# Kernel optimization log

Hardware: AMD Instinct MI355X
Metric: run time of the kernel (lower is better)

The kernel has to match this reference:

```python
import jax, jax.numpy as jnp
import numpy as np

WZ, WH, WW = 2, 6, 12          # window_size
NW = 64                        # type_of_windows = (8//2)*(96//6)
HEADS = 12
DIM = 384
B_ = 15                        # batch(1) * num_lon_windows(180//12)
N = WZ * WH * WW               # 144 tokens per window


def _construct_position_index():
    zi = np.arange(WZ); zj = -np.arange(WZ) * WZ
    hi = np.arange(WH); hj = -np.arange(WH) * WH
    w = np.arange(WW)
    c1 = np.stack(np.meshgrid(zi, hi, w, indexing='ij')).reshape(3, -1)
    c2 = np.stack(np.meshgrid(zj, hj, w, indexing='ij')).reshape(3, -1)
    coords = (c1[:, :, None] - c2[:, None, :]).transpose(1, 2, 0)  # (N, N, 3)
    coords[..., 2] += WW - 1
    coords[..., 1] *= 2 * WW - 1
    coords[..., 0] *= (2 * WW - 1) * WH * WH
    return coords.sum(-1).reshape(-1).astype(np.int32)  # (N*N,)


def setup_inputs() -> dict:
    key = jax.random.key(0)
    ks = jax.random.split(key, 6)
    bias_rows = (2 * WW - 1) * WH * WH * WZ * WZ  # 3312
    return {
        'x': jax.random.normal(ks[0], (B_, NW, N, DIM), dtype=jnp.float32),
        'mask': jnp.zeros((B_, N, N), dtype=jnp.float32),
        'w_qkv': jax.random.normal(ks[1], (DIM, 3 * DIM), dtype=jnp.float32) * 0.02,
        'b_qkv': jnp.zeros((3 * DIM,), dtype=jnp.float32),
        'w_proj': jax.random.normal(ks[2], (DIM, DIM), dtype=jnp.float32) * 0.02,
        'b_proj': jnp.zeros((DIM,), dtype=jnp.float32),
        'bias_table': jax.random.normal(ks[3], (bias_rows, NW, HEADS), dtype=jnp.float32) * 0.02,
        'position_index': jnp.asarray(_construct_position_index()),
    }


def reference(x, mask, w_qkv, b_qkv, w_proj, b_proj, bias_table, position_index):
    b_, nw, n, c = x.shape
    hd = c // HEADS
    scale = hd ** -0.5
    qkv = (x @ w_qkv + b_qkv).reshape(b_, nw, n, 3, HEADS, hd)
    q, k, v = jnp.moveaxis(qkv, 3, 0)            # each (B_, nW, N, H, hd)
    attn = jnp.einsum('bwnhd,bwmhd->bwhnm', q * scale, k)  # (B_, nW, H, N, N)
    # earth-specific relative bias gather: (N*N, nW, H) -> (nW, H, N, N)
    bias = bias_table[position_index].reshape(n, n, nw, HEADS).transpose(2, 3, 0, 1)
    attn = attn + bias[None]                     # broadcast over B_
    attn = attn + mask[:, None, None, :, :]      # additive mask per lon window
    attn = jax.nn.softmax(attn, axis=-1)         # dropout_rate=0 -> identity
    out = jnp.einsum('bwhnm,bwmhd->bwnhd', attn, v).reshape(b_, nw, n, c)
    return out @ w_proj + b_proj
```

## Files before the change

### kernel.cpp

```cpp
#include <hip/hip_runtime.h>
#include <cstdint>


typedef _Float16 f16;
typedef _Float16 f16x8 __attribute__((ext_vector_type(8)));
typedef _Float16 f16x4v __attribute__((ext_vector_type(4)));
typedef float f32x4 __attribute__((ext_vector_type(4)));

#define NW_ 64
#define HEADS_ 12
#define DIM_ 384
#define BATCH_ 15
#define NTOK_ 144
#define HD_ 32
#define MTOK_ (BATCH_*NW_*NTOK_)
#define NWH_ (BATCH_*NW_*HEADS_)

__device__ __forceinline__ void load16_lds(const void* g, void* l) {
    __builtin_amdgcn_global_load_lds(
        (const __attribute__((address_space(1))) uint32_t*)g,
        (__attribute__((address_space(3))) uint32_t*)l,
        16, 0, 0);
}

__device__ __forceinline__ f32x4 fzero4() {
    f32x4 z; z[0]=0.f; z[1]=0.f; z[2]=0.f; z[3]=0.f; return z;
}

__global__ void cvt_f32_to_f16(const float* __restrict__ src, f16* __restrict__ dst, int n4) {
    int i = blockIdx.x * blockDim.x + threadIdx.x;
    int stride = gridDim.x * blockDim.x;
    for (; i < n4; i += stride) {
        float4 v = ((const float4*)src)[i];
        f16x4v o;
        o[0] = (f16)v.x; o[1] = (f16)v.y; o[2] = (f16)v.z; o[3] = (f16)v.w;
        *(f16x4v*)(dst + 4*(size_t)i) = o;
    }
}

__global__ void transpose_cvt(const float* __restrict__ src, f16* __restrict__ dst, int K, int N) {
    int i = blockIdx.x * blockDim.x + threadIdx.x;
    if (i >= K*N) return;
    int n = i / K;
    int k = i - n*K;
    dst[i] = (f16)src[k*N + n];
}

__global__ __launch_bounds__(256) void qkv_gemm(
    const f16* __restrict__ A, const f16* __restrict__ Bt,
    const float* __restrict__ bias,
    f16* __restrict__ qws, f16* __restrict__ kws, f16* __restrict__ vws)
{
    constexpr int BK = 32;
    __shared__ __align__(16) f16 Asm[128*BK];
    __shared__ __align__(16) f16 Bsm[128*BK];
    const int tid  = threadIdx.x;
    const int lane = tid & 63;
    const int wave = tid >> 6;
    const int l15  = lane & 15;
    const int quad = lane >> 4;
    const int wr = wave >> 1, wc = wave & 1;
    const int row0 = blockIdx.x * 128;
    const int col0 = blockIdx.y * 128;

    f32x4 acc[4][4];
    #pragma unroll
    for (int i = 0; i < 4; ++i)
        #pragma unroll
        for (int j = 0; j < 4; ++j) acc[i][j] = fzero4();

    for (int kt = 0; kt < DIM_/BK; ++kt) {
        const int k0 = kt * BK;
        __syncthreads();
        #pragma unroll
        for (int cc = 0; cc < 2; ++cc) {
            int chunk  = wave*2 + cc;
            int flat16 = chunk*64 + lane;
            int r   = flat16 >> 2;
            int c16 = flat16 & 3;
            load16_lds(&A [(size_t)(row0 + r)*DIM_ + k0 + c16*8], (char*)Asm + (size_t)chunk*1024);
            load16_lds(&Bt[(size_t)(col0 + r)*DIM_ + k0 + c16*8], (char*)Bsm + (size_t)chunk*1024);
        }
        __syncthreads();

        f16x8 af[4], bf[4];
        #pragma unroll
        for (int i = 0; i < 4; ++i)
            af[i] = *(const f16x8*)&Asm[(wr*64 + i*16 + l15)*BK + quad*8];
        #pragma unroll
        for (int j = 0; j < 4; ++j)
            bf[j] = *(const f16x8*)&Bsm[(wc*64 + j*16 + l15)*BK + quad*8];
        #pragma unroll
        for (int i = 0; i < 4; ++i)
            #pragma unroll
            for (int j = 0; j < 4; ++j)
                acc[i][j] = __builtin_amdgcn_mfma_f32_16x16x32_f16(af[i], bf[j], acc[i][j], 0, 0, 0);
    }

    const int which = col0 / DIM_;
    #pragma unroll
    for (int j = 0; j < 4; ++j) {
        int col = col0 + wc*64 + j*16 + l15;
        float bq = bias[col];
        int rem = col - which*DIM_;
        int h = rem >> 5, d = rem & 31;
        #pragma unroll
        for (int i = 0; i < 4; ++i) {
            int rowb = row0 + wr*64 + i*16 + quad*4;
            #pragma unroll
            for (int r = 0; r < 4; ++r) {
                int row = rowb + r;
                int bw  = row / NTOK_;
                int n   = row - bw*NTOK_;
                int head = bw*HEADS_ + h;
                f16 hv = (f16)(acc[i][j][r] + bq);
                if (which == 0)      qws[(size_t)head*NTOK_*HD_ + n*HD_ + d] = hv;
                else if (which == 1) kws[(size_t)head*NTOK_*HD_ + n*HD_ + d] = hv;
                else                 vws[(size_t)head*HD_*NTOK_ + d*NTOK_ + n] = hv;
            }
        }
    }
}

__global__ __launch_bounds__(576) void attention(
    const f16* __restrict__ qws, const f16* __restrict__ kws, const f16* __restrict__ vws,
    const float* __restrict__ bias_table, const int* __restrict__ pos_idx,
    const float* __restrict__ mask, f16* __restrict__ ows)
{
    constexpr int KPAD = 40;
    constexpr int VPAD = 168;
    __shared__ __align__(16) char smem[10752 + 48384];
    f16* Vt  = (f16*)smem;
    f16* Ksm = (f16*)(smem + 10752);
    f16* Pst = (f16*)(smem + 10752);

    const int tid  = threadIdx.x;
    const int lane = tid & 63;
    const int wv   = tid >> 6;
    const int l15  = lane & 15;
    const int quad = lane >> 4;

    const int wh = blockIdx.x;
    const int w  = wh / HEADS_;
    const int h  = wh - w*HEADS_;

    float brg[9][4];
    #pragma unroll
    for (int j = 0; j < 9; ++j) {
        int m = j*16 + l15;
        #pragma unroll
        for (int r = 0; r < 4; ++r) {
            int n = wv*16 + quad*4 + r;
            int idx = pos_idx[n*NTOK_ + m];
            brg[j][r] = bias_table[(size_t)idx*(NW_*HEADS_) + w*HEADS_ + h];
        }
    }

    if (tid < 64) {
        int d = tid >> 1, m0 = 144 + (tid & 1)*8;
        uint4 z = {0u,0u,0u,0u};
        *(uint4*)&Vt[d*VPAD + m0] = z;
    }

    const float scale = 0.17677669529663687f;

    for (int b = 0; b < BATCH_; ++b) {
        const int bwh = (b*NW_ + w)*HEADS_ + h;
        const f16* qh = qws + (size_t)bwh*NTOK_*HD_;
        const f16* kh = kws + (size_t)bwh*NTOK_*HD_;
        const f16* vh = vws + (size_t)bwh*HD_*NTOK_;

        __syncthreads();
        {
            int flat = tid*8;
            int n = flat >> 5, d = flat & 31;
            *(uint4*)&Ksm[n*KPAD + d] = *(const uint4*)&kh[flat];
            int dv = flat / NTOK_;
            int mv = flat - dv*NTOK_;
            *(uint4*)&Vt[dv*VPAD + mv] = *(const uint4*)&vh[flat];
        }
        int nq = wv*16 + l15;
        f16x8 qf = *(const f16x8*)&qh[nq*HD_ + quad*8];
        __syncthreads();

        f32x4 sfr[9];
        #pragma unroll
        for (int j = 0; j < 9; ++j) {
            f16x8 kf = *(const f16x8*)&Ksm[(j*16 + l15)*KPAD + quad*8];
            sfr[j] = __builtin_amdgcn_mfma_f32_16x16x32_f16(qf, kf, fzero4(), 0, 0, 0);
        }
        __syncthreads();

        float p[9][4], rmax[4], rsum[4];
        #pragma unroll
        for (int r = 0; r < 4; ++r) rmax[r] = -1e30f;
        const float* mrow = mask + (size_t)b*NTOK_*NTOK_;
        #pragma unroll
        for (int j = 0; j < 9; ++j) {
            int m = j*16 + l15;
            #pragma unroll
            for (int r = 0; r < 4; ++r) {
                int n = wv*16 + quad*4 + r;
                float s = sfr[j][r]*scale + brg[j][r] + mrow[n*NTOK_ + m];
                p[j][r] = s;
                rmax[r] = fmaxf(rmax[r], s);
            }
        }
        #pragma unroll
        for (int r = 0; r < 4; ++r) {
            float v = rmax[r];
            #pragma unroll
            for (int off = 1; off < 16; off <<= 1)
                v = fmaxf(v, __shfl_xor(v, off, 64));
            rmax[r] = v;
        }
        #pragma unroll
        for (int r = 0; r < 4; ++r) rsum[r] = 0.f;
        #pragma unroll
        for (int j = 0; j < 9; ++j)
            #pragma unroll
            for (int r = 0; r < 4; ++r) {
                float e = __expf(p[j][r] - rmax[r]);
                p[j][r] = e;
                rsum[r] += e;
            }
        #pragma unroll
        for (int r = 0; r < 4; ++r) {
            float v = rsum[r];
            #pragma unroll
            for (int off = 1; off < 16; off <<= 1)
                v += __shfl_xor(v, off, 64);
            rsum[r] = 1.0f / v;
        }

        f16* Pw = Pst + wv*16*VPAD;
        #pragma unroll
        for (int j = 0; j < 9; ++j) {
            int m = j*16 + l15;
            #pragma unroll
            for (int r = 0; r < 4; ++r)
                Pw[(quad*4 + r)*VPAD + m] = (f16)(p[j][r]*rsum[r]);
        }
        if (lane < 32) {
            int row = lane >> 1, m0 = 144 + (lane & 1)*8;
            uint4 z = {0u,0u,0u,0u};
            *(uint4*)&Pw[row*VPAD + m0] = z;
        }

        f32x4 o0 = fzero4(), o1 = fzero4();
        #pragma unroll
        for (int s = 0; s < 5; ++s) {
            f16x8 pa = *(const f16x8*)&Pw[l15*VPAD + s*32 + quad*8];
            f16x8 v0 = *(const f16x8*)&Vt[l15*VPAD + s*32 + quad*8];
            f16x8 v1 = *(const f16x8*)&Vt[(16 + l15)*VPAD + s*32 + quad*8];
            o0 = __builtin_amdgcn_mfma_f32_16x16x32_f16(pa, v0, o0, 0, 0, 0);
            o1 = __builtin_amdgcn_mfma_f32_16x16x32_f16(pa, v1, o1, 0, 0, 0);
        }

        const int bw = b*NW_ + w;
        #pragma unroll
        for (int r = 0; r < 4; ++r) {
            int n = wv*16 + quad*4 + r;
            size_t base = ((size_t)bw*NTOK_ + n)*DIM_ + h*HD_;
            ows[base + l15]      = (f16)o0[r];
            ows[base + 16 + l15] = (f16)o1[r];
        }
    }
}

__global__ __launch_bounds__(256) void proj_gemm(
    const f16* __restrict__ A, const f16* __restrict__ Bt,
    const float* __restrict__ bias, float* __restrict__ out)
{
    constexpr int BK = 32;
    __shared__ __align__(16) f16 Asm[128*BK];
    __shared__ __align__(16) f16 Bsm[128*BK];
    const int tid  = threadIdx.x;
    const int lane = tid & 63;
    const int wave = tid >> 6;
    const int l15  = lane & 15;
    const int quad = lane >> 4;
    const int wr = wave >> 1, wc = wave & 1;
    const int row0 = blockIdx.x * 128;
    const int col0 = blockIdx.y * 128;

    f32x4 acc[4][4];
    #pragma unroll
    for (int i = 0; i < 4; ++i)
        #pragma unroll
        for (int j = 0; j < 4; ++j) acc[i][j] = fzero4();

    for (int kt = 0; kt < DIM_/BK; ++kt) {
        const int k0 = kt * BK;
        __syncthreads();
        #pragma unroll
        for (int cc = 0; cc < 2; ++cc) {
            int chunk  = wave*2 + cc;
            int flat16 = chunk*64 + lane;
            int r   = flat16 >> 2;
            int c16 = flat16 & 3;
            load16_lds(&A [(size_t)(row0 + r)*DIM_ + k0 + c16*8], (char*)Asm + (size_t)chunk*1024);
            load16_lds(&Bt[(size_t)(col0 + r)*DIM_ + k0 + c16*8], (char*)Bsm + (size_t)chunk*1024);
        }
        __syncthreads();

        f16x8 af[4], bf[4];
        #pragma unroll
        for (int i = 0; i < 4; ++i)
            af[i] = *(const f16x8*)&Asm[(wr*64 + i*16 + l15)*BK + quad*8];
        #pragma unroll
        for (int j = 0; j < 4; ++j)
            bf[j] = *(const f16x8*)&Bsm[(wc*64 + j*16 + l15)*BK + quad*8];
        #pragma unroll
        for (int i = 0; i < 4; ++i)
            #pragma unroll
            for (int j = 0; j < 4; ++j)
                acc[i][j] = __builtin_amdgcn_mfma_f32_16x16x32_f16(af[i], bf[j], acc[i][j], 0, 0, 0);
    }

    #pragma unroll
    for (int j = 0; j < 4; ++j) {
        int col = col0 + wc*64 + j*16 + l15;
        float bp = bias[col];
        #pragma unroll
        for (int i = 0; i < 4; ++i) {
            int rowb = row0 + wr*64 + i*16 + quad*4;
            #pragma unroll
            for (int r = 0; r < 4; ++r)
                out[(size_t)(rowb + r)*DIM_ + col] = acc[i][j][r] + bp;
        }
    }
}

extern "C" void kernel_launch(void* const* d_in, const int* in_sizes, int n_in,
                              void* d_out, int out_size, void* d_ws, size_t ws_size,
                              hipStream_t stream)
{
    const float* x      = (const float*)d_in[0];
    const float* mask   = (const float*)d_in[1];
    const float* w_qkv  = (const float*)d_in[2];
    const float* b_qkv  = (const float*)d_in[3];
    const float* w_proj = (const float*)d_in[4];
    const float* b_proj = (const float*)d_in[5];
    const float* btab   = (const float*)d_in[6];
    const int*   pidx   = (const int*)d_in[7];
    float* out = (float*)d_out;

    constexpr size_t X16_B = (size_t)MTOK_*DIM_*2;
    constexpr size_t WTQ_B = (size_t)1152*384*2;
    constexpr size_t WTP_B = (size_t)384*384*2;
    constexpr size_t HEAD_B = (size_t)NWH_*NTOK_*HD_*2;

    char* ws = (char*)d_ws;
    f16* x16 = (f16*)ws;
    f16* wtq = (f16*)(ws + X16_B);
    f16* wtp = (f16*)(ws + X16_B + WTQ_B);
    f16* qws = (f16*)(ws + X16_B + WTQ_B + WTP_B);
    f16* kws = (f16*)((char*)qws + HEAD_B);
    f16* vws = (f16*)((char*)kws + HEAD_B);
    f16* ows = x16;

    cvt_f32_to_f16<<<8192, 256, 0, stream>>>(x, x16, MTOK_*DIM_/4);
    transpose_cvt<<<(384*1152 + 255)/256, 256, 0, stream>>>(w_qkv, wtq, 384, 1152);
    transpose_cvt<<<(384*384  + 255)/256, 256, 0, stream>>>(w_proj, wtp, 384, 384);
    qkv_gemm<<<dim3(MTOK_/128, 1152/128), 256, 0, stream>>>(x16, wtq, b_qkv, qws, kws, vws);
    attention<<<NW_*HEADS_, 576, 0, stream>>>(qws, kws, vws, btab, pidx, mask, ows);
    proj_gemm<<<dim3(MTOK_/128, DIM_/128), 256, 0, stream>>>(ows, wtp, b_proj, out);
}
```

Measured before the change: 1.069 ms.

## Fuse x conversion into QKV GEMM and keep A rows in registers

The separate f32-to-f16 conversion pass over x is removed; the QKV GEMM now reads fp32 x directly and converts it into register-resident A fragments covering the full K=384. Each block owns 128 rows and loops over all output column tiles, staging 64-column B slabs in padded LDS. The projection GEMM gets the same row-stationary structure. This removes one full read and write of the activation tensor and the repeated A loads across column tiles. In exchange it uses more registers for the A fragments, launches fewer blocks, and leaves B loads unpipelined.

```diff
diff --git a/kernel.cpp b/kernel.cpp
--- a/kernel.cpp
+++ b/kernel.cpp
@@ -4,7 +4,6 @@
 
 typedef _Float16 f16;
 typedef _Float16 f16x8 __attribute__((ext_vector_type(8)));
-typedef _Float16 f16x4v __attribute__((ext_vector_type(4)));
 typedef float f32x4 __attribute__((ext_vector_type(4)));
 
 #define NW_ 64
@@ -15,27 +14,10 @@
 #define HD_ 32
 #define MTOK_ (BATCH_*NW_*NTOK_)
 #define NWH_ (BATCH_*NW_*HEADS_)
-
-__device__ __forceinline__ void load16_lds(const void* g, void* l) {
-    __builtin_amdgcn_global_load_lds(
-        (const __attribute__((address_space(1))) uint32_t*)g,
-        (__attribute__((address_space(3))) uint32_t*)l,
-        16, 0, 0);
-}
+#define BSLAB 520
 
 __device__ __forceinline__ f32x4 fzero4() {
     f32x4 z; z[0]=0.f; z[1]=0.f; z[2]=0.f; z[3]=0.f; return z;
-}
-
-__global__ void cvt_f32_to_f16(const float* __restrict__ src, f16* __restrict__ dst, int n4) {
-    int i = blockIdx.x * blockDim.x + threadIdx.x;
-    int stride = gridDim.x * blockDim.x;
-    for (; i < n4; i += stride) {
-        float4 v = ((const float4*)src)[i];
-        f16x4v o;
-        o[0] = (f16)v.x; o[1] = (f16)v.y; o[2] = (f16)v.z; o[3] = (f16)v.w;
-        *(f16x4v*)(dst + 4*(size_t)i) = o;
-    }
 }
 
 __global__ void transpose_cvt(const float* __restrict__ src, f16* __restrict__ dst, int K, int N) {
@@ -46,77 +28,88 @@
     dst[i] = (f16)src[k*N + n];
 }
 
-__global__ __launch_bounds__(256) void qkv_gemm(
-    const f16* __restrict__ A, const f16* __restrict__ Bt,
+__global__ __launch_bounds__(256, 2) void qkv_gemm(
+    const float* __restrict__ X, const f16* __restrict__ Bt,
     const float* __restrict__ bias,
     f16* __restrict__ qws, f16* __restrict__ kws, f16* __restrict__ vws)
 {
-    constexpr int BK = 32;
-    __shared__ __align__(16) f16 Asm[128*BK];
-    __shared__ __align__(16) f16 Bsm[128*BK];
+    __shared__ __align__(16) f16 Bsm[48 * BSLAB];
     const int tid  = threadIdx.x;
     const int lane = tid & 63;
     const int wave = tid >> 6;
     const int l15  = lane & 15;
     const int quad = lane >> 4;
-    const int wr = wave >> 1, wc = wave & 1;
-    const int row0 = blockIdx.x * 128;
-    const int col0 = blockIdx.y * 128;
-
-    f32x4 acc[4][4];
+    const int row0 = blockIdx.x * 128 + wave * 32;
+
+    f16x8 af[2][12];
     #pragma unroll
-    for (int i = 0; i < 4; ++i)
-        #pragma unroll
-        for (int j = 0; j < 4; ++j) acc[i][j] = fzero4();
-
-    for (int kt = 0; kt < DIM_/BK; ++kt) {
-        const int k0 = kt * BK;
-        __syncthreads();
-        #pragma unroll
-        for (int cc = 0; cc < 2; ++cc) {
-            int chunk  = wave*2 + cc;
-            int flat16 = chunk*64 + lane;
-            int r   = flat16 >> 2;
-            int c16 = flat16 & 3;
-            load16_lds(&A [(size_t)(row0 + r)*DIM_ + k0 + c16*8], (char*)Asm + (size_t)chunk*1024);
-            load16_lds(&Bt[(size_t)(col0 + r)*DIM_ + k0 + c16*8], (char*)Bsm + (size_t)chunk*1024);
-        }
-        __syncthreads();
-
-        f16x8 af[4], bf[4];
-        #pragma unroll
-        for (int i = 0; i < 4; ++i)
-            af[i] = *(const f16x8*)&Asm[(wr*64 + i*16 + l15)*BK + quad*8];
-        #pragma unroll
-        for (int j = 0; j < 4; ++j)
-            bf[j] = *(const f16x8*)&Bsm[(wc*64 + j*16 + l15)*BK + quad*8];
-        #pragma unroll
-        for (int i = 0; i < 4; ++i)
+    for (int i = 0; i < 2; ++i) {
+        const float* rp = &X[(size_t)(row0 + i*16 + l15)*DIM_ + quad*8];
+        #pragma unroll
+        for (int kt = 0; kt < 12; ++kt) {
+            float4 v0 = *(const float4*)(rp + kt*32);
+            float4 v1 = *(const float4*)(rp + kt*32 + 4);
+            f16x8 a;
+            a[0]=(f16)v0.x; a[1]=(f16)v0.y; a[2]=(f16)v0.z; a[3]=(f16)v0.w;
+            a[4]=(f16)v1.x; a[5]=(f16)v1.y; a[6]=(f16)v1.z; a[7]=(f16)v1.w;
+            af[i][kt] = a;
+        }
+    }
+
+    for (int ct = 0; ct < 18; ++ct) {
+        __syncthreads();
+        const f16* bsrc = Bt + (size_t)ct*64*DIM_;
+        #pragma unroll
+        for (int s = 0; s < 12; ++s) {
+            int flat = tid + s*256;
+            int r = flat / 48;
+            int c = flat - r*48;
+            f16x8 v = *(const f16x8*)&bsrc[(size_t)r*DIM_ + c*8];
+            *(f16x8*)&Bsm[c*BSLAB + r*8] = v;
+        }
+        __syncthreads();
+
+        f32x4 acc[2][4];
+        #pragma unroll
+        for (int i = 0; i < 2; ++i)
+            #pragma unroll
+            for (int j = 0; j < 4; ++j) acc[i][j] = fzero4();
+
+        #pragma unroll
+        for (int kt = 0; kt < 12; ++kt) {
+            f16x8 bf[4];
             #pragma unroll
             for (int j = 0; j < 4; ++j)
-                acc[i][j] = __builtin_amdgcn_mfma_f32_16x16x32_f16(af[i], bf[j], acc[i][j], 0, 0, 0);
-    }
-
-    const int which = col0 / DIM_;
-    #pragma unroll
-    for (int j = 0; j < 4; ++j) {
-        int col = col0 + wc*64 + j*16 + l15;
-        float bq = bias[col];
-        int rem = col - which*DIM_;
-        int h = rem >> 5, d = rem & 31;
-        #pragma unroll
-        for (int i = 0; i < 4; ++i) {
-            int rowb = row0 + wr*64 + i*16 + quad*4;
-            #pragma unroll
-            for (int r = 0; r < 4; ++r) {
-                int row = rowb + r;
-                int bw  = row / NTOK_;
-                int n   = row - bw*NTOK_;
-                int head = bw*HEADS_ + h;
-                f16 hv = (f16)(acc[i][j][r] + bq);
-                if (which == 0)      qws[(size_t)head*NTOK_*HD_ + n*HD_ + d] = hv;
-                else if (which == 1) kws[(size_t)head*NTOK_*HD_ + n*HD_ + d] = hv;
-                else                 vws[(size_t)head*HD_*NTOK_ + d*NTOK_ + n] = hv;
+                bf[j] = *(const f16x8*)&Bsm[(kt*4 + quad)*BSLAB + (j*16 + l15)*8];
+            #pragma unroll
+            for (int i = 0; i < 2; ++i)
+                #pragma unroll
+                for (int j = 0; j < 4; ++j)
+                    acc[i][j] = __builtin_amdgcn_mfma_f32_16x16x32_f16(af[i][kt], bf[j], acc[i][j], 0, 0, 0);
+        }
+
+        const int which = ct / 6;
+        const int cb = ct*64 - which*DIM_;
+        #pragma unroll
+        for (int j = 0; j < 4; ++j) {
+            int col = ct*64 + j*16 + l15;
+            float bq = bias[col];
+            int rem = cb + j*16 + l15;
+            int h = rem >> 5, d = rem & 31;
+            #pragma unroll
+            for (int i = 0; i < 2; ++i) {
+                int rowb = row0 + i*16 + quad*4;
+                #pragma unroll
+                for (int r = 0; r < 4; ++r) {
+                    int row = rowb + r;
+                    int bw  = row / NTOK_;
+                    int n   = row - bw*NTOK_;
+                    int head = bw*HEADS_ + h;
+                    f16 hv = (f16)(acc[i][j][r] + bq);
+                    if (which == 0)      qws[(size_t)head*NTOK_*HD_ + n*HD_ + d] = hv;
+                    else if (which == 1) kws[(size_t)head*NTOK_*HD_ + n*HD_ + d] = hv;
+                    else                 vws[(size_t)head*HD_*NTOK_ + d*NTOK_ + n] = hv;
+                }
             }
         }
     }
@@ -268,66 +261,70 @@
     }
 }
 
-__global__ __launch_bounds__(256) void proj_gemm(
+__global__ __launch_bounds__(256, 2) void proj_gemm(
     const f16* __restrict__ A, const f16* __restrict__ Bt,
     const float* __restrict__ bias, float* __restrict__ out)
 {
-    constexpr int BK = 32;
-    __shared__ __align__(16) f16 Asm[128*BK];
-    __shared__ __align__(16) f16 Bsm[128*BK];
+    __shared__ __align__(16) f16 Bsm[48 * BSLAB];
     const int tid  = threadIdx.x;
     const int lane = tid & 63;
     const int wave = tid >> 6;
     const int l15  = lane & 15;
     const int quad = lane >> 4;
-    const int wr = wave >> 1, wc = wave & 1;
-    const int row0 = blockIdx.x * 128;
-    const int col0 = blockIdx.y * 128;
-
-    f32x4 acc[4][4];
+    const int row0 = blockIdx.x * 128 + wave * 32;
+
+    f16x8 af[2][12];
     #pragma unroll
-    for (int i = 0; i < 4; ++i)
-        #pragma unroll
-        for (int j = 0; j < 4; ++j) acc[i][j] = fzero4();
-
-    for (int kt = 0; kt < DIM_/BK; ++kt) {
-        const int k0 = kt * BK;
-        __syncthreads();
-        #pragma unroll
-        for (int cc = 0; cc < 2; ++cc) {
-            int chunk  = wave*2 + cc;
-            int flat16 = chunk*64 + lane;
-            int r   = flat16 >> 2;
-            int c16 = flat16 & 3;
-            load16_lds(&A [(size_t)(row0 + r)*DIM_ + k0 + c16*8], (char*)Asm + (size_t)chunk*1024);
-            load16_lds(&Bt[(size_t)(col0 + r)*DIM_ + k0 + c16*8], (char*)Bsm + (size_t)chunk*1024);
-        }
-        __syncthreads();
-
-        f16x8 af[4], bf[4];
-        #pragma unroll
-        for (int i = 0; i < 4; ++i)
-            af[i] = *(const f16x8*)&Asm[(wr*64 + i*16 + l15)*BK + quad*8];
-        #pragma unroll
-        for (int j = 0; j < 4; ++j)
-            bf[j] = *(const f16x8*)&Bsm[(wc*64 + j*16 + l15)*BK + quad*8];
-        #pragma unroll
-        for (int i = 0; i < 4; ++i)
+    for (int i = 0; i < 2; ++i) {
+        const f16* rp = &A[(size_t)(row0 + i*16 + l15)*DIM_ + quad*8];
+        #pragma unroll
+        for (int kt = 0; kt < 12; ++kt)
+            af[i][kt] = *(const f16x8*)(rp + kt*32);
+    }
+
+    for (int ct = 0; ct < 6; ++ct) {
+        __syncthreads();
+        const f16* bsrc = Bt + (size_t)ct*64*DIM_;
+        #pragma unroll
+        for (int s = 0; s < 12; ++s) {
+            int flat = tid + s*256;
+            int r = flat / 48;
+            int c = flat - r*48;
+            f16x8 v = *(const f16x8*)&bsrc[(size_t)r*DIM_ + c*8];
+            *(f16x8*)&Bsm[c*BSLAB + r*8] = v;
+        }
+        __syncthreads();
+
+        f32x4 acc[2][4];
+        #pragma unroll
+        for (int i = 0; i < 2; ++i)
+            #pragma unroll
+            for (int j = 0; j < 4; ++j) acc[i][j] = fzero4();
+
+        #pragma unroll
+        for (int kt = 0; kt < 12; ++kt) {
+            f16x8 bf[4];
             #pragma unroll
             for (int j = 0; j < 4; ++j)
-                acc[i][j] = __builtin_amdgcn_mfma_f32_16x16x32_f16(af[i], bf[j], acc[i][j], 0, 0, 0);
-    }
-
-    #pragma unroll
-    for (int j = 0; j < 4; ++j) {
-        int col = col0 + wc*64 + j*16 + l15;
-        float bp = bias[col];
-        #pragma unroll
-        for (int i = 0; i < 4; ++i) {
-            int rowb = row0 + wr*64 + i*16 + quad*4;
-            #pragma unroll
-            for (int r = 0; r < 4; ++r)
-                out[(size_t)(rowb + r)*DIM_ + col] = acc[i][j][r] + bp;
+                bf[j] = *(const f16x8*)&Bsm[(kt*4 + quad)*BSLAB + (j*16 + l15)*8];
+            #pragma unroll
+            for (int i = 0; i < 2; ++i)
+                #pragma unroll
+                for (int j = 0; j < 4; ++j)
+                    acc[i][j] = __builtin_amdgcn_mfma_f32_16x16x32_f16(af[i][kt], bf[j], acc[i][j], 0, 0, 0);
+        }
+
+        #pragma unroll
+        for (int j = 0; j < 4; ++j) {
+            int col = ct*64 + j*16 + l15;
+            float bp = bias[col];
+            #pragma unroll
+            for (int i = 0; i < 2; ++i) {
+                int rowb = row0 + i*16 + quad*4;
+                #pragma unroll
+                for (int r = 0; r < 4; ++r)
+                    out[(size_t)(rowb + r)*DIM_ + col] = acc[i][j][r] + bp;
+            }
         }
     }
 }
@@ -346,24 +343,22 @@
     const int*   pidx   = (const int*)d_in[7];
     float* out = (float*)d_out;
 
-    constexpr size_t X16_B = (size_t)MTOK_*DIM_*2;
+    constexpr size_t OWS_B = (size_t)MTOK_*DIM_*2;
     constexpr size_t WTQ_B = (size_t)1152*384*2;
     constexpr size_t WTP_B = (size_t)384*384*2;
     constexpr size_t HEAD_B = (size_t)NWH_*NTOK_*HD_*2;
 
     char* ws = (char*)d_ws;
-    f16* x16 = (f16*)ws;
-    f16* wtq = (f16*)(ws + X16_B);
-    f16* wtp = (f16*)(ws + X16_B + WTQ_B);
-    f16* qws = (f16*)(ws + X16_B + WTQ_B + WTP_B);
+    f16* ows = (f16*)ws;
+    f16* wtq = (f16*)(ws + OWS_B);
+    f16* wtp = (f16*)(ws + OWS_B + WTQ_B);
+    f16* qws = (f16*)(ws + OWS_B + WTQ_B + WTP_B);
     f16* kws = (f16*)((char*)qws + HEAD_B);
     f16* vws = (f16*)((char*)kws + HEAD_B);
-    f16* ows = x16;
-
-    cvt_f32_to_f16<<<8192, 256, 0, stream>>>(x, x16, MTOK_*DIM_/4);
+
     transpose_cvt<<<(384*1152 + 255)/256, 256, 0, stream>>>(w_qkv, wtq, 384, 1152);
     transpose_cvt<<<(384*384  + 255)/256, 256, 0, stream>>>(w_proj, wtp, 384, 384);
-    qkv_gemm<<<dim3(MTOK_/128, 1152/128), 256, 0, stream>>>(x16, wtq, b_qkv, qws, kws, vws);
+    qkv_gemm<<<MTOK_/128, 256, 0, stream>>>(x, wtq, b_qkv, qws, kws, vws);
     attention<<<NW_*HEADS_, 576, 0, stream>>>(qws, kws, vws, btab, pidx, mask, ows);
-    proj_gemm<<<dim3(MTOK_/128, DIM_/128), 256, 0, stream>>>(ows, wtp, b_proj, out);
-}
+    proj_gemm<<<MTOK_/128, 256, 0, stream>>>(ows, wtp, b_proj, out);
+}
```

New measurement: 1.242 ms. 1.16x slower.
